# Optimization experiments

Measured on AMD Instinct MI355X. Metric: run time of the kernel, lower is better.

Reference implementation:

```python
import jax, jax.numpy as jnp
import numpy as np

NUM_GROUPS = 32
EPS = 1e-05
HT_MIN = -1.0
HT_MAX = 1.0


def setup_inputs() -> dict:
    key = jax.random.key(0)
    k1, k2, k3 = jax.random.split(key, 3)
    B, IN, OUT = 4096, 2048, 2048
    x = jax.random.normal(k1, (B, IN), dtype=jnp.float32)
    # kaiming-uniform-ish scale for weight, uniform bias bound 1/sqrt(in)
    weight = jax.random.normal(k2, (OUT, IN), dtype=jnp.float32) * (1.0 / np.sqrt(IN))
    bias = jax.random.uniform(k3, (OUT,), dtype=jnp.float32, minval=-1.0 / np.sqrt(IN), maxval=1.0 / np.sqrt(IN))
    gn_weight = jnp.ones((OUT,), dtype=jnp.float32)
    gn_bias = jnp.zeros((OUT,), dtype=jnp.float32)
    return {"x": x, "weight": weight, "bias": bias, "gn_weight": gn_weight, "gn_bias": gn_bias}


def reference(x, weight, bias, gn_weight, gn_bias):
    # Linear: y = x @ W^T + b   -> [B, OUT]
    y = jnp.einsum("bi,oi->bo", x, weight) + bias
    B, C = y.shape
    G = NUM_GROUPS
    yg = y.reshape(B, G, C // G)
    mean = jnp.mean(yg, axis=-1, keepdims=True)
    var = jnp.mean(jnp.square(yg), axis=-1, keepdims=True) - jnp.square(mean)
    yn = ((yg - mean) * jax.lax.rsqrt(var + EPS)).reshape(B, C)
    out = yn * gn_weight + gn_bias
    return jnp.clip(out, HT_MIN, HT_MAX)
```

## Files before the change

kernel.cpp:

```cpp
#include <hip/hip_runtime.h>
#include <stdint.h>

#define B_ROWS 4096
#define C_OUT  2048
#define C_IN   2048
#define EPS    1e-5f

typedef __attribute__((ext_vector_type(8))) short bf16x8;
typedef __attribute__((ext_vector_type(4))) float f32x4;

__device__ __forceinline__ unsigned short f2bf(float f) {
    uint32_t u = __float_as_uint(f);
    uint32_t r = (u + 0x7fffu + ((u >> 16) & 1u)) >> 16;
    return (unsigned short)r;
}

__global__ void cvt_f32_bf16_kernel(const float* __restrict__ x,
                                    const float* __restrict__ w,
                                    unsigned short* __restrict__ xb,
                                    unsigned short* __restrict__ wb,
                                    int nx4, int nw4) {
    int i = blockIdx.x * blockDim.x + threadIdx.x;
    const float* src;
    unsigned short* dst;
    if (i < nx4) {
        src = x; dst = xb;
    } else {
        i -= nx4;
        if (i >= nw4) return;
        src = w; dst = wb;
    }
    float4 v = ((const float4*)src)[i];
    ushort4 o;
    o.x = f2bf(v.x); o.y = f2bf(v.y); o.z = f2bf(v.z); o.w = f2bf(v.w);
    ((ushort4*)dst)[i] = o;
}

__global__ __launch_bounds__(512, 4)
void gemm_gn_kernel(const unsigned short* __restrict__ A,
                    const unsigned short* __restrict__ W,
                    const float* __restrict__ bias,
                    const float* __restrict__ gnw,
                    const float* __restrict__ gnb,
                    float* __restrict__ out) {
    __shared__ __align__(16) unsigned short smem[2 * 16384];

    const int bc   = blockIdx.x;
    const int br   = blockIdx.y;
    const int t    = threadIdx.x;
    const int lane = t & 63;
    const int wave = t >> 6;
    const int wr   = wave & 1;
    const int wc   = (wave >> 1) & 1;
    const int kh   = wave >> 2;
    const int c16  = lane & 15;
    const int quad = lane >> 4;

    f32x4 acc[4][4];
#pragma unroll
    for (int i = 0; i < 4; i++)
#pragma unroll
        for (int j = 0; j < 4; j++) acc[i][j] = (f32x4){0.f, 0.f, 0.f, 0.f};

    const int r0 = t >> 3;
    const int qo = ((t & 7) ^ (r0 & 7)) * 8;
    const unsigned short* gA = A + (size_t)(br * 128 + r0) * C_IN + qo;
    const unsigned short* gB = W + (size_t)(bc * 128 + r0) * C_IN + qo;

#define STAGE(buf, k0)                                                                     \
    do {                                                                                   \
        unsigned short* sa = smem + (buf) * 16384;                                         \
        unsigned short* sb = sa + 8192;                                                    \
        _Pragma("unroll")                                                                  \
        for (int n = 0; n < 2; n++)                                                        \
            __builtin_amdgcn_global_load_lds(                                              \
                (const __attribute__((address_space(1))) void*)(gA + (size_t)(n * 64) * C_IN + (k0)), \
                (__attribute__((address_space(3))) void*)(sa + n * 4096 + t * 8), 16, 0, 0); \
        _Pragma("unroll")                                                                  \
        for (int n = 0; n < 2; n++)                                                        \
            __builtin_amdgcn_global_load_lds(                                              \
                (const __attribute__((address_space(1))) void*)(gB + (size_t)(n * 64) * C_IN + (k0)), \
                (__attribute__((address_space(3))) void*)(sb + n * 4096 + t * 8), 16, 0, 0); \
    } while (0)

    const int qs = (((kh << 2) | quad) ^ (c16 & 7)) * 8;

    STAGE(0, 0);
    int cur = 0;
    for (int it = 0; it < 32; ++it) {
        __syncthreads();
        if (it < 31) STAGE(cur ^ 1, (it + 1) * 64);

        const unsigned short* sa = smem + cur * 16384;
        const unsigned short* sb = sa + 8192;
        bf16x8 a[4], b[4];
#pragma unroll
        for (int i = 0; i < 4; i++)
            a[i] = *(const bf16x8*)(sa + (wr * 64 + i * 16 + c16) * 64 + qs);
#pragma unroll
        for (int j = 0; j < 4; j++)
            b[j] = *(const bf16x8*)(sb + (wc * 64 + j * 16 + c16) * 64 + qs);
#pragma unroll
        for (int i = 0; i < 4; i++)
#pragma unroll
            for (int j = 0; j < 4; j++)
                acc[i][j] = __builtin_amdgcn_mfma_f32_16x16x32_bf16(a[i], b[j], acc[i][j], 0, 0, 0);
        cur ^= 1;
    }

    __syncthreads();
    float* fbuf = (float*)smem;
    if (kh == 1) {
#pragma unroll
        for (int i = 0; i < 4; i++)
#pragma unroll
            for (int j = 0; j < 4; j++)
                *(f32x4*)(fbuf + (wave & 3) * 4096 + i * 1024 + j * 256 + lane * 4) = acc[i][j];
    }
    __syncthreads();
    if (kh == 1) return;
#pragma unroll
    for (int i = 0; i < 4; i++)
#pragma unroll
        for (int j = 0; j < 4; j++)
            acc[i][j] += *(const f32x4*)(fbuf + (wave & 3) * 4096 + i * 1024 + j * 256 + lane * 4);

    const int colbase = bc * 128 + wc * 64;
    const int rowbase = br * 128 + wr * 64;
    float bv[4], gw[4], gb[4];
#pragma unroll
    for (int j = 0; j < 4; j++) {
        int col = colbase + j * 16 + c16;
        bv[j] = bias[col];
        gw[j] = gnw[col];
        gb[j] = gnb[col];
    }
#pragma unroll
    for (int i = 0; i < 4; i++) {
#pragma unroll
        for (int r = 0; r < 4; r++) {
            float s = 0.f, ss = 0.f;
#pragma unroll
            for (int j = 0; j < 4; j++) {
                float v = acc[i][j][r] + bv[j];
                acc[i][j][r] = v;
                s += v;
                ss += v * v;
            }
#pragma unroll
            for (int m = 1; m < 16; m <<= 1) {
                s  += __shfl_xor(s, m, 64);
                ss += __shfl_xor(ss, m, 64);
            }
            float mean = s * (1.f / 64.f);
            float var  = ss * (1.f / 64.f) - mean * mean;
            float rstd = rsqrtf(var + EPS);
            int row = rowbase + i * 16 + quad * 4 + r;
            float* orow = out + (size_t)row * C_OUT;
#pragma unroll
            for (int j = 0; j < 4; j++) {
                float v = (acc[i][j][r] - mean) * rstd * gw[j] + gb[j];
                v = fminf(1.f, fmaxf(-1.f, v));
                orow[colbase + j * 16 + c16] = v;
            }
        }
    }
}

extern "C" void kernel_launch(void* const* d_in, const int* in_sizes, int n_in,
                              void* d_out, int out_size, void* d_ws, size_t ws_size,
                              hipStream_t stream) {
    const float* x    = (const float*)d_in[0];
    const float* w    = (const float*)d_in[1];
    const float* bias = (const float*)d_in[2];
    const float* gnw  = (const float*)d_in[3];
    const float* gnb  = (const float*)d_in[4];
    float* out = (float*)d_out;

    unsigned short* xb = (unsigned short*)d_ws;
    unsigned short* wb = xb + (size_t)B_ROWS * C_IN;

    const int nx4 = B_ROWS * C_IN / 4;
    const int nw4 = C_OUT * C_IN / 4;
    cvt_f32_bf16_kernel<<<(nx4 + nw4 + 255) / 256, 256, 0, stream>>>(x, w, xb, wb, nx4, nw4);

    dim3 grid(C_OUT / 128, B_ROWS / 128);
    gemm_gn_kernel<<<grid, 512, 0, stream>>>(xb, wb, bias, gnw, gnb, out);
}
```

Baseline: 136.1 us.

## Use 256x128 tiles with triple-buffered LDS pipeline and drop split-K reduction

Enlarges the block tile to 256 rows by 128 columns so that each of the eight waves owns a distinct 64x64 output sub-tile. This removes the intra-block split-K and its LDS reduction. LDS staging becomes a three-buffer ring with loads issued in halves, explicit vmcnt waits, raw s_barrier, and setprio around the MFMA bursts, so global loads overlap compute two stages ahead. The larger tile increases reuse of operands loaded from global memory, but it halves the grid to 256 blocks, uses more LDS, and lowers the occupancy target.

```diff
diff --git a/kernel.cpp b/kernel.cpp
--- a/kernel.cpp
+++ b/kernel.cpp
@@ -36,23 +36,22 @@
     ((ushort4*)dst)[i] = o;
 }
 
-__global__ __launch_bounds__(512, 4)
+__global__ __launch_bounds__(512, 2)
 void gemm_gn_kernel(const unsigned short* __restrict__ A,
                     const unsigned short* __restrict__ W,
                     const float* __restrict__ bias,
                     const float* __restrict__ gnw,
                     const float* __restrict__ gnb,
                     float* __restrict__ out) {
-    __shared__ __align__(16) unsigned short smem[2 * 16384];
+    __shared__ __align__(16) unsigned short smem[3 * 24576];
 
     const int bc   = blockIdx.x;
     const int br   = blockIdx.y;
-    const int t    = threadIdx.x;
-    const int lane = t & 63;
-    const int wave = t >> 6;
-    const int wr   = wave & 1;
-    const int wc   = (wave >> 1) & 1;
-    const int kh   = wave >> 2;
+    const int tid  = threadIdx.x;
+    const int lane = tid & 63;
+    const int wave = tid >> 6;
+    const int wr   = wave >> 1;
+    const int wc   = wave & 1;
     const int c16  = lane & 15;
     const int quad = lane >> 4;
 
@@ -62,71 +61,97 @@
 #pragma unroll
         for (int j = 0; j < 4; j++) acc[i][j] = (f32x4){0.f, 0.f, 0.f, 0.f};
 
-    const int r0 = t >> 3;
-    const int qo = ((t & 7) ^ (r0 & 7)) * 8;
-    const unsigned short* gA = A + (size_t)(br * 128 + r0) * C_IN + qo;
+    const int r0 = tid >> 3;
+    const int qo = ((tid & 7) ^ (r0 & 7)) * 8;
+    const unsigned short* gA = A + (size_t)(br * 256 + r0) * C_IN + qo;
     const unsigned short* gB = W + (size_t)(bc * 128 + r0) * C_IN + qo;
-
-#define STAGE(buf, k0)                                                                     \
-    do {                                                                                   \
-        unsigned short* sa = smem + (buf) * 16384;                                         \
-        unsigned short* sb = sa + 8192;                                                    \
-        _Pragma("unroll")                                                                  \
-        for (int n = 0; n < 2; n++)                                                        \
-            __builtin_amdgcn_global_load_lds(                                              \
+    const int t8 = tid * 8;
+
+#define STAGE_H(dst, k0, half)                                                                      \
+    do {                                                                                            \
+        _Pragma("unroll")                                                                           \
+        for (int n = (half) * 2; n < (half) * 2 + 2; n++)                                           \
+            __builtin_amdgcn_global_load_lds(                                                       \
                 (const __attribute__((address_space(1))) void*)(gA + (size_t)(n * 64) * C_IN + (k0)), \
-                (__attribute__((address_space(3))) void*)(sa + n * 4096 + t * 8), 16, 0, 0); \
-        _Pragma("unroll")                                                                  \
-        for (int n = 0; n < 2; n++)                                                        \
-            __builtin_amdgcn_global_load_lds(                                              \
-                (const __attribute__((address_space(1))) void*)(gB + (size_t)(n * 64) * C_IN + (k0)), \
-                (__attribute__((address_space(3))) void*)(sb + n * 4096 + t * 8), 16, 0, 0); \
+                (__attribute__((address_space(3))) void*)((dst) + n * 4096 + t8), 16, 0, 0);        \
+        __builtin_amdgcn_global_load_lds(                                                           \
+            (const __attribute__((address_space(1))) void*)(gB + (size_t)((half) * 64) * C_IN + (k0)), \
+            (__attribute__((address_space(3))) void*)((dst) + 16384 + (half) * 4096 + t8), 16, 0, 0); \
     } while (0)
 
-    const int qs = (((kh << 2) | quad) ^ (c16 & 7)) * 8;
-
-    STAGE(0, 0);
-    int cur = 0;
-    for (int it = 0; it < 32; ++it) {
-        __syncthreads();
-        if (it < 31) STAGE(cur ^ 1, (it + 1) * 64);
-
-        const unsigned short* sa = smem + cur * 16384;
-        const unsigned short* sb = sa + 8192;
-        bf16x8 a[4], b[4];
+    unsigned short* bf0 = smem;
+    unsigned short* bf1 = smem + 24576;
+    unsigned short* bf2 = smem + 49152;
+
+    STAGE_H(bf0, 0, 0);  STAGE_H(bf0, 0, 1);
+    STAGE_H(bf1, 64, 0); STAGE_H(bf1, 64, 1);
+    asm volatile("s_waitcnt vmcnt(6)" ::: "memory");
+    __builtin_amdgcn_s_barrier();
+
+    const unsigned short* pr = bf0;
+    const unsigned short* pn = bf1;
+    unsigned short*       ps = bf2;
+
+#pragma unroll 1
+    for (int kt = 0; kt < 32; ++kt) {
+        const int k2 = (kt + 2) * 64;
+        bf16x8 a[4], bq[4];
+
+        {
+            const int qs = (quad ^ (c16 & 7)) * 8;
+#pragma unroll
+            for (int i = 0; i < 4; i++)
+                a[i] = *(const bf16x8*)(pr + (wr * 64 + i * 16 + c16) * 64 + qs);
+#pragma unroll
+            for (int j = 0; j < 4; j++)
+                bq[j] = *(const bf16x8*)(pr + 16384 + (wc * 64 + j * 16 + c16) * 64 + qs);
+        }
+        if (kt < 30) STAGE_H(ps, k2, 0);
+        __builtin_amdgcn_s_barrier();
+        asm volatile("s_waitcnt lgkmcnt(0)" ::: "memory");
+        __builtin_amdgcn_sched_barrier(0);
+        __builtin_amdgcn_s_setprio(1);
 #pragma unroll
         for (int i = 0; i < 4; i++)
-            a[i] = *(const bf16x8*)(sa + (wr * 64 + i * 16 + c16) * 64 + qs);
-#pragma unroll
-        for (int j = 0; j < 4; j++)
-            b[j] = *(const bf16x8*)(sb + (wc * 64 + j * 16 + c16) * 64 + qs);
+#pragma unroll
+            for (int j = 0; j < 4; j++)
+                acc[i][j] = __builtin_amdgcn_mfma_f32_16x16x32_bf16(a[i], bq[j], acc[i][j], 0, 0, 0);
+        __builtin_amdgcn_s_setprio(0);
+        __builtin_amdgcn_s_barrier();
+
+        {
+            const int qs = ((4 + quad) ^ (c16 & 7)) * 8;
+#pragma unroll
+            for (int i = 0; i < 4; i++)
+                a[i] = *(const bf16x8*)(pr + (wr * 64 + i * 16 + c16) * 64 + qs);
+#pragma unroll
+            for (int j = 0; j < 4; j++)
+                bq[j] = *(const bf16x8*)(pr + 16384 + (wc * 64 + j * 16 + c16) * 64 + qs);
+        }
+        if (kt < 30) STAGE_H(ps, k2, 1);
+        __builtin_amdgcn_s_barrier();
+        asm volatile("s_waitcnt lgkmcnt(0)" ::: "memory");
+        __builtin_amdgcn_sched_barrier(0);
+        __builtin_amdgcn_s_setprio(1);
 #pragma unroll
         for (int i = 0; i < 4; i++)
 #pragma unroll
             for (int j = 0; j < 4; j++)
-                acc[i][j] = __builtin_amdgcn_mfma_f32_16x16x32_bf16(a[i], b[j], acc[i][j], 0, 0, 0);
-        cur ^= 1;
-    }
-
-    __syncthreads();
-    float* fbuf = (float*)smem;
-    if (kh == 1) {
-#pragma unroll
-        for (int i = 0; i < 4; i++)
-#pragma unroll
-            for (int j = 0; j < 4; j++)
-                *(f32x4*)(fbuf + (wave & 3) * 4096 + i * 1024 + j * 256 + lane * 4) = acc[i][j];
-    }
-    __syncthreads();
-    if (kh == 1) return;
-#pragma unroll
-    for (int i = 0; i < 4; i++)
-#pragma unroll
-        for (int j = 0; j < 4; j++)
-            acc[i][j] += *(const f32x4*)(fbuf + (wave & 3) * 4096 + i * 1024 + j * 256 + lane * 4);
+                acc[i][j] = __builtin_amdgcn_mfma_f32_16x16x32_bf16(a[i], bq[j], acc[i][j], 0, 0, 0);
+        __builtin_amdgcn_s_setprio(0);
+
+        if (kt < 30)       asm volatile("s_waitcnt vmcnt(6)" ::: "memory");
+        else if (kt == 30) asm volatile("s_waitcnt vmcnt(0)" ::: "memory");
+        __builtin_amdgcn_s_barrier();
+
+        const unsigned short* tmp = pr;
+        pr = pn;
+        pn = ps;
+        ps = (unsigned short*)tmp;
+    }
 
     const int colbase = bc * 128 + wc * 64;
-    const int rowbase = br * 128 + wr * 64;
+    const int rowbase = br * 256 + wr * 64;
     float bv[4], gw[4], gb[4];
 #pragma unroll
     for (int j = 0; j < 4; j++) {
@@ -184,6 +209,6 @@
     const int nw4 = C_OUT * C_IN / 4;
     cvt_f32_bf16_kernel<<<(nx4 + nw4 + 255) / 256, 256, 0, stream>>>(x, w, xb, wb, nx4, nw4);
 
-    dim3 grid(C_OUT / 128, B_ROWS / 128);
+    dim3 grid(C_OUT / 128, B_ROWS / 256);
     gemm_gn_kernel<<<grid, 512, 0, stream>>>(xb, wb, bias, gnw, gnb, out);
 }
```

After: 140.2 us. 1.03x slower.
